# Kernel optimization log

Hardware: AMD Instinct MI355X
Metric: run time of the kernel (lower is better)

The kernel has to match this reference:

```python
import jax, jax.numpy as jnp
import numpy as np

# ---- HashGridPlanesEncoder config (hybrid-k-planes) ----
NUM_LEVELS = 16
LEVEL_DIM = 2
BASE_RES = 16
DESIRED_RES = 2048
LOG2_HASHMAP = 19
D = 2  # grid_nd: each plane encoder is a 2D hash grid
N_PTS = 1048576
COO_COMBS = [(0, 1), (0, 2), (1, 2)]
HASH_PRIME_1 = 2654435761  # torch-ngp fast_hash prime for dim 1 (dim 0 prime is 1)


def _level_constants():
    # Mirrors torch-ngp GridEncoder offset/resolution computation.
    pls = 2.0 ** (np.log2(DESIRED_RES / BASE_RES) / (NUM_LEVELS - 1))
    max_params = 2 ** LOG2_HASHMAP
    scales, res, sizes, offs = [], [], [], [0]
    for l in range(NUM_LEVELS):
        s = BASE_RES * pls ** l - 1.0          # kernel: scale = exp2(l*S + H) - 1
        r = int(np.ceil(s)) + 1                # kernel: resolution = ceil(scale) + 1
        p = min(max_params, (r + 1) ** D)      # align_corners=False -> (res+1)^D
        p = int(np.ceil(p / 8) * 8)            # round up to multiple of 8
        scales.append(s); res.append(r); sizes.append(p); offs.append(offs[-1] + p)
    return (np.array(scales, np.float32), np.array(res, np.int64),
            np.array(sizes, np.int64), np.array(offs[:-1], np.int64), offs[-1])


SCALES, RES, SIZES, OFFSETS, TOTAL_PARAMS = _level_constants()
USE_HASH = ((RES + 1) ** D) > SIZES  # static per-level: dense linear index vs spatial hash


def _encode_plane(x2, table):
    """x2: [N,2] coords in [0,1]; table: [TOTAL_PARAMS, LEVEL_DIM]. Returns [N, L*C]."""
    n = x2.shape[0]
    scales = jnp.asarray(SCALES)
    pos = x2[:, None, :] * scales[None, :, None] + 0.5           # [N,L,2] (align_corners=False)
    pg_f = jnp.floor(pos)
    frac = pos - pg_f                                            # [N,L,2]
    pg = pg_f.astype(jnp.uint32)
    corners = jnp.array([[0, 0], [1, 0], [0, 1], [1, 1]], jnp.uint32)  # [4,2]
    cpos = pg[:, :, None, :] + corners[None, None]               # [N,L,4,2]
    cmask = corners.astype(bool)[None, None]                     # [1,1,4,2]
    w = jnp.where(cmask, frac[:, :, None, :], 1.0 - frac[:, :, None, :]).prod(-1)  # [N,L,4]
    stride1 = jnp.asarray((RES + 1).astype(np.uint32))           # [L]
    linear = cpos[..., 0] + cpos[..., 1] * stride1[None, :, None]
    hashed = cpos[..., 0] ^ (cpos[..., 1] * jnp.uint32(HASH_PRIME_1))  # uint32 wrap-around
    idx = jnp.where(jnp.asarray(USE_HASH)[None, :, None], hashed, linear)
    idx = idx % jnp.asarray(SIZES.astype(np.uint32))[None, :, None]
    idx = (idx + jnp.asarray(OFFSETS.astype(np.uint32))[None, :, None]).astype(jnp.int32)
    feats = table[idx]                                           # [N,L,4,C] gather
    out = (w[..., None] * feats).sum(axis=2)                     # [N,L,C] bilinear interp
    return out.reshape(n, NUM_LEVELS * LEVEL_DIM)


def setup_inputs() -> dict:
    key = jax.random.key(0)
    kp, k0, k1, k2 = jax.random.split(key, 4)
    pts = jax.random.uniform(kp, (N_PTS, 3), dtype=jnp.float32)  # coords (treated as in [-1,1] domain)
    std = 1e-4  # GridEncoder init: embeddings.uniform_(-1e-4, 1e-4)
    mk = lambda k: jax.random.uniform(k, (TOTAL_PARAMS, LEVEL_DIM), jnp.float32, -std, std)
    return {"pts": pts, "table_xy": mk(k0), "table_xz": mk(k1), "table_yz": mk(k2)}


def reference(pts, table_xy, table_xz, table_yz):
    # GridEncoder.forward normalizes inputs: (x + bound) / (2*bound), bound=1
    u = (pts + 1.0) * 0.5
    tables = (table_xy, table_xz, table_yz)
    out = _encode_plane(u[:, list(COO_COMBS[0])], tables[0])
    for comb, tab in zip(COO_COMBS[1:], tables[1:]):
        out = out + _encode_plane(u[:, list(comb)], tab)
    return out
```

## Files before the change

### kernel.cpp

```cpp
#include <hip/hip_runtime.h>
#include <hip/hip_fp16.h>
#include <cmath>

#define NLEV 16
#define HASH_START 12
#define HMASK ((1u << 19) - 1u)
#define HASH_PRIME 2654435761u
#define LDS_WORDS 14160

typedef float    f4 __attribute__((ext_vector_type(4)));
typedef unsigned u4 __attribute__((ext_vector_type(4)));

struct LvlC {
  float scale[NLEV];
  unsigned stride[NLEV];
  unsigned offset[NLEV];
};

__device__ __forceinline__ float2 h2f(unsigned u) {
  return __half22float2(__builtin_bit_cast(__half2, u));
}

__global__ __launch_bounds__(256) void k_convert(
    const float2* __restrict__ t0, const float2* __restrict__ t1,
    const float2* __restrict__ t2, unsigned* __restrict__ dst, unsigned total)
{
  unsigned g = blockIdx.x * 256 + threadIdx.x;
  unsigned stp = gridDim.x * 256;
  unsigned tot3 = 3u * total;
  for (unsigned e = g; e < tot3; e += stp) {
    const float2* src; unsigned i = e;
    if (i < total)            { src = t0; }
    else if (i < 2u * total)  { src = t1; i -= total; }
    else                      { src = t2; i -= 2u * total; }
    float2 v = src[i];
    __half2 h = __floats2half2_rn(v.x, v.y);
    __builtin_nontemporal_store(__builtin_bit_cast(unsigned, h), dst + e);
  }
}

__device__ __forceinline__ void hash_row(
    const unsigned* __restrict__ tp, unsigned x0, unsigned hy,
    unsigned& g0, unsigned& g1)
{
  unsigned a0 = (x0 ^ hy) & HMASK;
  if ((x0 & 1u) == 0u) {
    uint2 v = *reinterpret_cast<const uint2*>(tp + (a0 & ~1u));
    bool hi = (a0 & 1u) != 0u;
    g0 = hi ? v.y : v.x;
    g1 = hi ? v.x : v.y;
  } else {
    g0 = tp[a0];
    g1 = tp[((x0 + 1u) ^ hy) & HMASK];
  }
}

__global__ __launch_bounds__(256) void k_hash_lvl(
    const float* __restrict__ pts, const unsigned* __restrict__ tab,
    unsigned* __restrict__ slice, float sc, unsigned o, unsigned total, int half)
{
  int t = blockIdx.x * 256 + threadIdx.x;
  if (t >= half) return;
  const int idx[2] = {t, t + half};

  float ua[2][3], ub[2][3];
#pragma unroll
  for (int k = 0; k < 2; ++k) {
    float u0 = (pts[3 * idx[k] + 0] + 1.f) * .5f;
    float u1 = (pts[3 * idx[k] + 1] + 1.f) * .5f;
    float u2 = (pts[3 * idx[k] + 2] + 1.f) * .5f;
    ua[k][0] = u0; ub[k][0] = u1;
    ua[k][1] = u0; ub[k][1] = u2;
    ua[k][2] = u1; ub[k][2] = u2;
  }

  unsigned g[2][3][4];
  float rx[2][3], ry[2][3];
#pragma unroll
  for (int k = 0; k < 2; ++k)
#pragma unroll
    for (int p = 0; p < 3; ++p) {
      float px = ua[k][p] * sc + .5f, py = ub[k][p] * sc + .5f;
      float fx = floorf(px), fy = floorf(py);
      rx[k][p] = px - fx; ry[k][p] = py - fy;
      unsigned x0 = (unsigned)fx, y0 = (unsigned)fy;
      unsigned hy0 = y0 * HASH_PRIME, hy1 = hy0 + HASH_PRIME;
      const unsigned* tp = tab + (size_t)p * total + o;
      hash_row(tp, x0, hy0, g[k][p][0], g[k][p][1]);
      hash_row(tp, x0, hy1, g[k][p][2], g[k][p][3]);
    }

#pragma unroll
  for (int k = 0; k < 2; ++k) {
    float s0 = 0.f, s1 = 0.f;
#pragma unroll
    for (int p = 0; p < 3; ++p) {
      float x = rx[k][p], y = ry[k][p];
      float w00 = (1.f - x) * (1.f - y), w10 = x * (1.f - y);
      float w01 = (1.f - x) * y,          w11 = x * y;
      float2 f00 = h2f(g[k][p][0]), f10 = h2f(g[k][p][1]);
      float2 f01 = h2f(g[k][p][2]), f11 = h2f(g[k][p][3]);
      s0 += w00 * f00.x + w10 * f10.x + w01 * f01.x + w11 * f11.x;
      s1 += w00 * f00.y + w10 * f10.y + w01 * f01.y + w11 * f11.y;
    }
    __builtin_nontemporal_store(
        __builtin_bit_cast(unsigned, __floats2half2_rn(s0, s1)), slice + idx[k]);
  }
}

__global__ __launch_bounds__(512) void k_final(
    const float* __restrict__ pts, const unsigned* __restrict__ tab,
    const unsigned* __restrict__ slices,
    float* __restrict__ out, LvlC lc, unsigned total, int n)
{
  __shared__ unsigned lds[LDS_WORDS];
  int i = blockIdx.x * 512 + threadIdx.x;

  float u0 = (pts[3 * i + 0] + 1.f) * .5f;
  float u1 = (pts[3 * i + 1] + 1.f) * .5f;
  float u2 = (pts[3 * i + 2] + 1.f) * .5f;
  const float ua[3] = {u0, u0, u1}, ub[3] = {u1, u2, u2};

  float res[24];
#pragma unroll
  for (int j = 0; j < 12; ++j) res[j] = 0.f;

  uint2 g[2][3][2];
  float gx[2][3], gy[2][3];

#pragma unroll 1
  for (int p = 0; p < 3; ++p) {
    if (p) __syncthreads();
    const u4* src = reinterpret_cast<const u4*>(tab + (size_t)p * total);
    for (unsigned e = threadIdx.x; e < LDS_WORDS / 4; e += 512)
      reinterpret_cast<u4*>(lds)[e] = src[e];
#pragma unroll
    for (int h = 0; h < 2; ++h) {
      const int l = 6 + 2 * p + h;
      const float sc = lc.scale[l];
      const unsigned st = lc.stride[l], o = lc.offset[l];
#pragma unroll
      for (int q = 0; q < 3; ++q) {
        float px = ua[q] * sc + .5f, py = ub[q] * sc + .5f;
        float fx = floorf(px), fy = floorf(py);
        gx[h][q] = px - fx; gy[h][q] = py - fy;
        unsigned i00 = (unsigned)fx + (unsigned)fy * st + o;
        const unsigned* tp = tab + (size_t)q * total;
        g[h][q][0] = *reinterpret_cast<const uint2*>(tp + i00);
        g[h][q][1] = *reinterpret_cast<const uint2*>(tp + i00 + st);
      }
    }
    __syncthreads();
#pragma unroll
    for (int l = 0; l < 6; ++l) {
      const float sc = lc.scale[l];
      const unsigned st = lc.stride[l], o = lc.offset[l];
      float px = ua[p] * sc + .5f, py = ub[p] * sc + .5f;
      float fx = floorf(px), fy = floorf(py);
      float x = px - fx, y = py - fy;
      unsigned i00 = (unsigned)fx + (unsigned)fy * st + o;
      float2 f00 = h2f(lds[i00]),      f10 = h2f(lds[i00 + 1]);
      float2 f01 = h2f(lds[i00 + st]), f11 = h2f(lds[i00 + st + 1]);
      float w00 = (1.f - x) * (1.f - y), w10 = x * (1.f - y);
      float w01 = (1.f - x) * y,          w11 = x * y;
      res[2 * l + 0] += w00 * f00.x + w10 * f10.x + w01 * f01.x + w11 * f11.x;
      res[2 * l + 1] += w00 * f00.y + w10 * f10.y + w01 * f01.y + w11 * f11.y;
    }
#pragma unroll
    for (int h = 0; h < 2; ++h) {
      float s0 = 0.f, s1 = 0.f;
#pragma unroll
      for (int q = 0; q < 3; ++q) {
        float x = gx[h][q], y = gy[h][q];
        float w00 = (1.f - x) * (1.f - y), w10 = x * (1.f - y);
        float w01 = (1.f - x) * y,          w11 = x * y;
        float2 f00 = h2f(g[h][q][0].x), f10 = h2f(g[h][q][0].y);
        float2 f01 = h2f(g[h][q][1].x), f11 = h2f(g[h][q][1].y);
        s0 += w00 * f00.x + w10 * f10.x + w01 * f01.x + w11 * f11.x;
        s1 += w00 * f00.y + w10 * f10.y + w01 * f01.y + w11 * f11.y;
      }
      res[12 + 4 * p + 2 * h + 0] = s0;
      res[12 + 4 * p + 2 * h + 1] = s1;
    }
  }

  unsigned sl[4];
#pragma unroll
  for (int j = 0; j < 4; ++j) sl[j] = slices[(size_t)j * n + i];

  float v[32];
#pragma unroll
  for (int j = 0; j < 24; ++j) v[j] = res[j];
#pragma unroll
  for (int j = 0; j < 4; ++j) {
    float2 f = h2f(sl[j]);
    v[24 + 2 * j] = f.x; v[24 + 2 * j + 1] = f.y;
  }
  float4* o4 = (float4*)(out + (size_t)i * 32);
#pragma unroll
  for (int j = 0; j < 8; ++j)
    o4[j] = make_float4(v[4 * j], v[4 * j + 1], v[4 * j + 2], v[4 * j + 3]);
}

__global__ __launch_bounds__(256) void k_fallback(
    const float* __restrict__ pts, const float2* __restrict__ txy,
    const float2* __restrict__ txz, const float2* __restrict__ tyz,
    float* __restrict__ out, LvlC lc, int n)
{
  int i = blockIdx.x * 256 + threadIdx.x;
  if (i >= n) return;
  float u0 = (pts[3 * i + 0] + 1.f) * .5f;
  float u1 = (pts[3 * i + 1] + 1.f) * .5f;
  float u2 = (pts[3 * i + 2] + 1.f) * .5f;
  const float ua[3] = {u0, u0, u1}, ub[3] = {u1, u2, u2};
  const float2* tabs[3] = {txy, txz, tyz};
  float acc[32];
#pragma unroll
  for (int j = 0; j < 32; ++j) acc[j] = 0.f;
#pragma unroll
  for (int l = 0; l < NLEV; ++l) {
    const float sc = lc.scale[l];
    const unsigned o = lc.offset[l], s = lc.stride[l];
#pragma unroll
    for (int p = 0; p < 3; ++p) {
      const float2* t = tabs[p];
      float px = ua[p] * sc + .5f, py = ub[p] * sc + .5f;
      float fx = floorf(px), fy = floorf(py);
      float rx = px - fx, ry = py - fy;
      unsigned x0 = (unsigned)fx, y0 = (unsigned)fy;
      float w00 = (1.f - rx) * (1.f - ry), w10 = rx * (1.f - ry);
      float w01 = (1.f - rx) * ry,          w11 = rx * ry;
      float2 f00, f10, f01, f11;
      if (l >= HASH_START) {
        unsigned hy0 = y0 * HASH_PRIME, hy1 = hy0 + HASH_PRIME;
        f00 = t[o + ((x0 ^ hy0) & HMASK)];
        f10 = t[o + (((x0 + 1u) ^ hy0) & HMASK)];
        f01 = t[o + ((x0 ^ hy1) & HMASK)];
        f11 = t[o + (((x0 + 1u) ^ hy1) & HMASK)];
      } else {
        unsigned i00 = x0 + y0 * s;
        float4 r0 = *reinterpret_cast<const float4*>(t + o + i00);
        float4 r1 = *reinterpret_cast<const float4*>(t + o + i00 + s);
        f00 = make_float2(r0.x, r0.y); f10 = make_float2(r0.z, r0.w);
        f01 = make_float2(r1.x, r1.y); f11 = make_float2(r1.z, r1.w);
      }
      acc[2 * l + 0] += w00 * f00.x + w10 * f10.x + w01 * f01.x + w11 * f11.x;
      acc[2 * l + 1] += w00 * f00.y + w10 * f10.y + w01 * f01.y + w11 * f11.y;
    }
  }
  float4* o4 = (float4*)(out + (size_t)i * 32);
#pragma unroll
  for (int j = 0; j < 8; ++j)
    o4[j] = make_float4(acc[4 * j], acc[4 * j + 1], acc[4 * j + 2], acc[4 * j + 3]);
}

static unsigned compute_levels(LvlC* lc)
{
  const double pls = std::pow(2.0, std::log2(2048.0 / 16.0) / 15.0);
  unsigned long long off = 0;
  for (int l = 0; l < NLEV; ++l) {
    double s = 16.0 * std::pow(pls, (double)l) - 1.0;
    lc->scale[l] = (float)s;
    long long r = (long long)std::ceil(s) + 1;
    long long dense = (r + 1) * (r + 1);
    long long sz = dense < (1LL << 19) ? dense : (1LL << 19);
    sz = ((sz + 7) / 8) * 8;
    lc->stride[l] = (unsigned)(r + 1);
    lc->offset[l] = (unsigned)off;
    off += (unsigned long long)sz;
  }
  return (unsigned)off;
}

extern "C" void kernel_launch(void* const* d_in, const int* in_sizes, int n_in,
                              void* d_out, int out_size, void* d_ws, size_t ws_size,
                              hipStream_t stream) {
  const float*  pts = (const float*)d_in[0];
  const float2* txy = (const float2*)d_in[1];
  const float2* txz = (const float2*)d_in[2];
  const float2* tyz = (const float2*)d_in[3];
  float* out = (float*)d_out;
  int n = in_sizes[0] / 3;

  LvlC lc;
  unsigned total = compute_levels(&lc);

  size_t tab_bytes = (size_t)3 * total * 4;
  size_t tab_al = (tab_bytes + 255) & ~(size_t)255;
  size_t need = tab_al + (size_t)4 * n * 4;

  bool ok = (n % 512 == 0) && (lc.offset[6] == LDS_WORDS) && (ws_size >= need);
  for (int l = HASH_START; l < NLEV; ++l) {
    unsigned sz = ((l + 1 < NLEV) ? lc.offset[l + 1] : total) - lc.offset[l];
    ok = ok && (sz == (1u << 19));
  }

  int block = 256;
  int grid = (n + block - 1) / block;
  if (!ok) {
    k_fallback<<<grid, block, 0, stream>>>(pts, txy, txz, tyz, out, lc, n);
    return;
  }

  unsigned* tab16 = (unsigned*)d_ws;
  unsigned* slices = (unsigned*)((char*)d_ws + tab_al);

  int half = n / 2;
  int gridh = half / block;

  k_convert<<<2048, 256, 0, stream>>>(txy, txz, tyz, tab16, total);
  for (int l = HASH_START; l < NLEV; ++l)
    k_hash_lvl<<<gridh, block, 0, stream>>>(pts, tab16, slices + (size_t)(l - 12) * n,
                                            lc.scale[l], lc.offset[l], total, half);
  k_final<<<n / 512, 512, 0, stream>>>(pts, tab16, slices, out, lc, total, n);
}
```

Baseline: 321.0 us.

## Fuse hash-level gathers into final kernel with software-pipelined issue/consume

Removes the four per-level hash kernels and their half-precision slice buffers, computing hashed levels 12-15 directly inside the final kernel. Hash gathers for the next level are issued before the LDS-phase work so their latency overlaps the dense and LDS interpolation. This avoids writing and rereading slice buffers and saves launches. In exchange the per-level locality that made the L2-resident hash table (one level of 3 planes at a time) cache-friendly is lost, since all four levels' tables are now touched concurrently, and register pressure rises.

After: 373.7 us. 1.16x slower.

```diff
diff --git a/kernel.cpp b/kernel.cpp
--- a/kernel.cpp
+++ b/kernel.cpp
@@ -55,62 +55,87 @@
   }
 }
 
-__global__ __launch_bounds__(256) void k_hash_lvl(
-    const float* __restrict__ pts, const unsigned* __restrict__ tab,
-    unsigned* __restrict__ slice, float sc, unsigned o, unsigned total, int half)
-{
-  int t = blockIdx.x * 256 + threadIdx.x;
-  if (t >= half) return;
-  const int idx[2] = {t, t + half};
-
-  float ua[2][3], ub[2][3];
-#pragma unroll
-  for (int k = 0; k < 2; ++k) {
-    float u0 = (pts[3 * idx[k] + 0] + 1.f) * .5f;
-    float u1 = (pts[3 * idx[k] + 1] + 1.f) * .5f;
-    float u2 = (pts[3 * idx[k] + 2] + 1.f) * .5f;
-    ua[k][0] = u0; ub[k][0] = u1;
-    ua[k][1] = u0; ub[k][1] = u2;
-    ua[k][2] = u1; ub[k][2] = u2;
-  }
-
-  unsigned g[2][3][4];
-  float rx[2][3], ry[2][3];
-#pragma unroll
-  for (int k = 0; k < 2; ++k)
-#pragma unroll
-    for (int p = 0; p < 3; ++p) {
-      float px = ua[k][p] * sc + .5f, py = ub[k][p] * sc + .5f;
-      float fx = floorf(px), fy = floorf(py);
-      rx[k][p] = px - fx; ry[k][p] = py - fy;
-      unsigned x0 = (unsigned)fx, y0 = (unsigned)fy;
-      unsigned hy0 = y0 * HASH_PRIME, hy1 = hy0 + HASH_PRIME;
-      const unsigned* tp = tab + (size_t)p * total + o;
-      hash_row(tp, x0, hy0, g[k][p][0], g[k][p][1]);
-      hash_row(tp, x0, hy1, g[k][p][2], g[k][p][3]);
-    }
-
-#pragma unroll
-  for (int k = 0; k < 2; ++k) {
+__device__ __forceinline__ void issue_dense(
+    const unsigned* __restrict__ tab, size_t total, const LvlC& lc, int l0,
+    const float* ua, const float* ub, uint2 (&g)[2][3][2])
+{
+#pragma unroll
+  for (int h = 0; h < 2; ++h) {
+    const float sc = lc.scale[l0 + h];
+    const unsigned st = lc.stride[l0 + h], o = lc.offset[l0 + h];
+#pragma unroll
+    for (int q = 0; q < 3; ++q) {
+      float px = ua[q] * sc + .5f, py = ub[q] * sc + .5f;
+      unsigned i00 = (unsigned)floorf(px) + (unsigned)floorf(py) * st + o;
+      const unsigned* tp = tab + (size_t)q * total;
+      g[h][q][0] = *reinterpret_cast<const uint2*>(tp + i00);
+      g[h][q][1] = *reinterpret_cast<const uint2*>(tp + i00 + st);
+    }
+  }
+}
+
+__device__ __forceinline__ void consume_dense(
+    const LvlC& lc, int l0, const float* ua, const float* ub,
+    const uint2 (&g)[2][3][2], float* res4)
+{
+#pragma unroll
+  for (int h = 0; h < 2; ++h) {
+    const float sc = lc.scale[l0 + h];
     float s0 = 0.f, s1 = 0.f;
 #pragma unroll
-    for (int p = 0; p < 3; ++p) {
-      float x = rx[k][p], y = ry[k][p];
+    for (int q = 0; q < 3; ++q) {
+      float px = ua[q] * sc + .5f, py = ub[q] * sc + .5f;
+      float x = px - floorf(px), y = py - floorf(py);
       float w00 = (1.f - x) * (1.f - y), w10 = x * (1.f - y);
       float w01 = (1.f - x) * y,          w11 = x * y;
-      float2 f00 = h2f(g[k][p][0]), f10 = h2f(g[k][p][1]);
-      float2 f01 = h2f(g[k][p][2]), f11 = h2f(g[k][p][3]);
+      float2 f00 = h2f(g[h][q][0].x), f10 = h2f(g[h][q][0].y);
+      float2 f01 = h2f(g[h][q][1].x), f11 = h2f(g[h][q][1].y);
       s0 += w00 * f00.x + w10 * f10.x + w01 * f01.x + w11 * f11.x;
       s1 += w00 * f00.y + w10 * f10.y + w01 * f01.y + w11 * f11.y;
     }
-    __builtin_nontemporal_store(
-        __builtin_bit_cast(unsigned, __floats2half2_rn(s0, s1)), slice + idx[k]);
-  }
+    res4[2 * h + 0] = s0; res4[2 * h + 1] = s1;
+  }
+}
+
+__device__ __forceinline__ void issue_hash1(
+    const unsigned* __restrict__ tab, size_t total, const LvlC& lc, int l,
+    const float* ua, const float* ub, unsigned (&g)[3][4])
+{
+  const float sc = lc.scale[l];
+  const unsigned o = lc.offset[l];
+#pragma unroll
+  for (int q = 0; q < 3; ++q) {
+    float px = ua[q] * sc + .5f, py = ub[q] * sc + .5f;
+    unsigned x0 = (unsigned)floorf(px), y0 = (unsigned)floorf(py);
+    unsigned hy0 = y0 * HASH_PRIME, hy1 = hy0 + HASH_PRIME;
+    const unsigned* tp = tab + (size_t)q * total + o;
+    hash_row(tp, x0, hy0, g[q][0], g[q][1]);
+    hash_row(tp, x0, hy1, g[q][2], g[q][3]);
+  }
+}
+
+__device__ __forceinline__ void consume_hash1(
+    const LvlC& lc, int l, const float* ua, const float* ub,
+    const unsigned (&g)[3][4], float* res2)
+{
+  const float sc = lc.scale[l];
+  float s0 = 0.f, s1 = 0.f;
+#pragma unroll
+  for (int q = 0; q < 3; ++q) {
+    float px = ua[q] * sc + .5f, py = ub[q] * sc + .5f;
+    float x = px - floorf(px), y = py - floorf(py);
+    float w00 = (1.f - x) * (1.f - y), w10 = x * (1.f - y);
+    float w01 = (1.f - x) * y,          w11 = x * y;
+    float2 f00 = h2f(g[q][0]), f10 = h2f(g[q][1]);
+    float2 f01 = h2f(g[q][2]), f11 = h2f(g[q][3]);
+    s0 += w00 * f00.x + w10 * f10.x + w01 * f01.x + w11 * f11.x;
+    s1 += w00 * f00.y + w10 * f10.y + w01 * f01.y + w11 * f11.y;
+  }
+  res2[0] = s0; res2[1] = s1;
 }
 
 __global__ __launch_bounds__(512) void k_final(
     const float* __restrict__ pts, const unsigned* __restrict__ tab,
-    const unsigned* __restrict__ slices,
     float* __restrict__ out, LvlC lc, unsigned total, int n)
 {
   __shared__ unsigned lds[LDS_WORDS];
@@ -121,12 +146,14 @@
   float u2 = (pts[3 * i + 2] + 1.f) * .5f;
   const float ua[3] = {u0, u0, u1}, ub[3] = {u1, u2, u2};
 
-  float res[24];
+  float res[32];
 #pragma unroll
   for (int j = 0; j < 12; ++j) res[j] = 0.f;
 
-  uint2 g[2][3][2];
-  float gx[2][3], gy[2][3];
+  uint2 gd[2][3][2];
+  unsigned gh[3][4];
+
+  issue_hash1(tab, total, lc, 12, ua, ub, gh);
 
 #pragma unroll 1
   for (int p = 0; p < 3; ++p) {
@@ -134,22 +161,7 @@
     const u4* src = reinterpret_cast<const u4*>(tab + (size_t)p * total);
     for (unsigned e = threadIdx.x; e < LDS_WORDS / 4; e += 512)
       reinterpret_cast<u4*>(lds)[e] = src[e];
-#pragma unroll
-    for (int h = 0; h < 2; ++h) {
-      const int l = 6 + 2 * p + h;
-      const float sc = lc.scale[l];
-      const unsigned st = lc.stride[l], o = lc.offset[l];
-#pragma unroll
-      for (int q = 0; q < 3; ++q) {
-        float px = ua[q] * sc + .5f, py = ub[q] * sc + .5f;
-        float fx = floorf(px), fy = floorf(py);
-        gx[h][q] = px - fx; gy[h][q] = py - fy;
-        unsigned i00 = (unsigned)fx + (unsigned)fy * st + o;
-        const unsigned* tp = tab + (size_t)q * total;
-        g[h][q][0] = *reinterpret_cast<const uint2*>(tp + i00);
-        g[h][q][1] = *reinterpret_cast<const uint2*>(tp + i00 + st);
-      }
-    }
+    issue_dense(tab, total, lc, 6 + 2 * p, ua, ub, gd);
     __syncthreads();
 #pragma unroll
     for (int l = 0; l < 6; ++l) {
@@ -166,40 +178,18 @@
       res[2 * l + 0] += w00 * f00.x + w10 * f10.x + w01 * f01.x + w11 * f11.x;
       res[2 * l + 1] += w00 * f00.y + w10 * f10.y + w01 * f01.y + w11 * f11.y;
     }
-#pragma unroll
-    for (int h = 0; h < 2; ++h) {
-      float s0 = 0.f, s1 = 0.f;
-#pragma unroll
-      for (int q = 0; q < 3; ++q) {
-        float x = gx[h][q], y = gy[h][q];
-        float w00 = (1.f - x) * (1.f - y), w10 = x * (1.f - y);
-        float w01 = (1.f - x) * y,          w11 = x * y;
-        float2 f00 = h2f(g[h][q][0].x), f10 = h2f(g[h][q][0].y);
-        float2 f01 = h2f(g[h][q][1].x), f11 = h2f(g[h][q][1].y);
-        s0 += w00 * f00.x + w10 * f10.x + w01 * f01.x + w11 * f11.x;
-        s1 += w00 * f00.y + w10 * f10.y + w01 * f01.y + w11 * f11.y;
-      }
-      res[12 + 4 * p + 2 * h + 0] = s0;
-      res[12 + 4 * p + 2 * h + 1] = s1;
-    }
-  }
-
-  unsigned sl[4];
-#pragma unroll
-  for (int j = 0; j < 4; ++j) sl[j] = slices[(size_t)j * n + i];
-
-  float v[32];
-#pragma unroll
-  for (int j = 0; j < 24; ++j) v[j] = res[j];
-#pragma unroll
-  for (int j = 0; j < 4; ++j) {
-    float2 f = h2f(sl[j]);
-    v[24 + 2 * j] = f.x; v[24 + 2 * j + 1] = f.y;
-  }
+    consume_dense(lc, 6 + 2 * p, ua, ub, gd, res + 12 + 4 * p);
+    consume_hash1(lc, 12 + p, ua, ub, gh, res + 24 + 2 * p);
+    if (p < 2) issue_hash1(tab, total, lc, 13 + p, ua, ub, gh);
+  }
+
+  issue_hash1(tab, total, lc, 15, ua, ub, gh);
+  consume_hash1(lc, 15, ua, ub, gh, res + 30);
+
   float4* o4 = (float4*)(out + (size_t)i * 32);
 #pragma unroll
   for (int j = 0; j < 8; ++j)
-    o4[j] = make_float4(v[4 * j], v[4 * j + 1], v[4 * j + 2], v[4 * j + 3]);
+    o4[j] = make_float4(res[4 * j], res[4 * j + 1], res[4 * j + 2], res[4 * j + 3]);
 }
 
 __global__ __launch_bounds__(256) void k_fallback(
@@ -285,9 +275,7 @@
   LvlC lc;
   unsigned total = compute_levels(&lc);
 
-  size_t tab_bytes = (size_t)3 * total * 4;
-  size_t tab_al = (tab_bytes + 255) & ~(size_t)255;
-  size_t need = tab_al + (size_t)4 * n * 4;
+  size_t need = (size_t)3 * total * 4;
 
   bool ok = (n % 512 == 0) && (lc.offset[6] == LDS_WORDS) && (ws_size >= need);
   for (int l = HASH_START; l < NLEV; ++l) {
@@ -303,14 +291,6 @@
   }
 
   unsigned* tab16 = (unsigned*)d_ws;
-  unsigned* slices = (unsigned*)((char*)d_ws + tab_al);
-
-  int half = n / 2;
-  int gridh = half / block;
-
   k_convert<<<2048, 256, 0, stream>>>(txy, txz, tyz, tab16, total);
-  for (int l = HASH_START; l < NLEV; ++l)
-    k_hash_lvl<<<gridh, block, 0, stream>>>(pts, tab16, slices + (size_t)(l - 12) * n,
-                                            lc.scale[l], lc.offset[l], total, half);
-  k_final<<<n / 512, 512, 0, stream>>>(pts, tab16, slices, out, lc, total, n);
-}
+  k_final<<<n / 512, 512, 0, stream>>>(pts, tab16, out, lc, total, n);
+}
```
